# Kernel optimization log

Measured on AMD Instinct MI355X. Metric: run time of the kernel, lower is better.

## Reference

```python
import jax, jax.numpy as jnp
import numpy as np

B, LC, LQ, D, F = 16, 2048, 256, 768, 768
MASK_VALUE = -1.0e12


def setup_inputs() -> dict:
    key = jax.random.key(0)
    ks = jax.random.split(key, 6)
    scale = 1.0 / np.sqrt(D)
    return {
        "x_cont": jax.random.normal(ks[0], (B, LC, D), dtype=jnp.float32),
        "x_ques": jax.random.normal(ks[1], (B, LQ, D), dtype=jnp.float32),
        "ques_len": jax.random.randint(ks[2], (B, 1), 0, LQ, dtype=jnp.int32),
        "WC": jax.random.normal(ks[3], (D, F), dtype=jnp.float32) * scale,
        "WQ": jax.random.normal(ks[4], (D, F), dtype=jnp.float32) * scale,
        "V": jax.random.normal(ks[5], (2 * D, F), dtype=jnp.float32) * scale,
    }


def _mask_logits(logits, ques_len):
    # Original: one_hot(ques_len[:,0], Lq) -> 1 - cumsum along Lq -> tile over Lc.
    # mask[b, j] = 1 if j < ques_len[b] else 0.
    lq = logits.shape[-1]
    oh = jax.nn.one_hot(ques_len[:, 0], lq, dtype=jnp.float32)  # [B, Lq]
    valid = 1.0 - jnp.cumsum(oh, axis=1)                         # [B, Lq]
    return logits + MASK_VALUE * (1.0 - valid)[:, None, :]       # broadcast over Lc


def reference(x_cont, x_ques, ques_len, WC, WQ, V):
    filters = WC.shape[-1]
    x_cont_ = jax.nn.relu(jnp.einsum("bcd,df->bcf", x_cont, WC))  # [B, Lc, F]
    x_ques_ = jax.nn.relu(jnp.einsum("bqd,df->bqf", x_ques, WQ))  # [B, Lq, F]
    logits = jnp.einsum("bcf,bqf->bcq", x_cont_, x_ques_) / jnp.sqrt(
        jnp.asarray(filters, dtype=x_cont.dtype)
    )  # [B, Lc, Lq]
    logits = _mask_logits(logits, ques_len)
    attn = jax.nn.softmax(logits, axis=-1)
    C = jnp.einsum("bcq,bqd->bcd", attn, x_ques)                  # [B, Lc, D]
    res = jnp.concatenate([x_cont, C], axis=2)                    # [B, Lc, 2D]
    gate = jax.nn.sigmoid(jnp.einsum("bce,ef->bcf", res, V))      # [B, Lc, F]
    return gate
```

## Files before the change

### kernel.cpp

```cpp
#include <hip/hip_runtime.h>
#include <hip/hip_bf16.h>
#include <cstdint>


using bf16 = __hip_bfloat16;
typedef __attribute__((ext_vector_type(8))) __bf16 bf16x8;
typedef __attribute__((ext_vector_type(4))) float f32x4;

typedef __attribute__((address_space(1))) const uint32_t GU32;
typedef __attribute__((address_space(3))) uint32_t LU32;

__device__ __forceinline__ void gll16(const bf16* g, bf16* l) {
  __builtin_amdgcn_global_load_lds((GU32*)g, (LU32*)l, 16, 0, 0);
}
__device__ __forceinline__ f32x4 mfma_bf16(bf16x8 a, bf16x8 b, f32x4 c) {
  return __builtin_amdgcn_mfma_f32_16x16x32_bf16(a, b, c, 0, 0, 0);
}
__device__ __forceinline__ bf16x8 ld_frag(const bf16* p) {
  return *reinterpret_cast<const bf16x8*>(p);
}
__device__ __forceinline__ int swz(int r) { return (r & 3) ^ ((r >> 2) & 1); }

__device__ __forceinline__ unsigned short f2bf_bits(float x) {
  bf16 b = __float2bfloat16(x);
  union { bf16 b; unsigned short s; } u;
  u.b = b;
  return u.s;
}

__global__ void transpose4(const float* __restrict__ s0, const float* __restrict__ s1,
                           const float* __restrict__ s2, const float* __restrict__ s3,
                           bf16* __restrict__ d0, bf16* __restrict__ d1,
                           bf16* __restrict__ d2, bf16* __restrict__ d3) {
  __shared__ float tile[32][33];
  const int z = blockIdx.z;
  const float* in = (z == 0) ? s0 : (z == 1) ? s1 : (z == 2) ? s2 : s3;
  bf16* out = (z == 0) ? d0 : (z == 1) ? d1 : (z == 2) ? d2 : d3;
  int c0 = blockIdx.x * 32, r0 = blockIdx.y * 32;
  int tx = threadIdx.x, ty = threadIdx.y;
#pragma unroll
  for (int i = ty; i < 32; i += 8)
    tile[i][tx] = in[(long)(r0 + i) * 768 + (c0 + tx)];
  __syncthreads();
#pragma unroll
  for (int i = ty; i < 32; i += 8)
    out[(long)(c0 + i) * 768 + (r0 + tx)] = __float2bfloat16(tile[tx][i]);
}

__global__ void transpose_bf16(const bf16* __restrict__ in, bf16* __restrict__ out,
                               int R, int C, long ibs, long obs) {
  __shared__ bf16 tile[32][33];
  const bf16* inb = in + (long)blockIdx.z * ibs;
  bf16* outb = out + (long)blockIdx.z * obs;
  int c0 = blockIdx.x * 32, r0 = blockIdx.y * 32;
  int tx = threadIdx.x, ty = threadIdx.y;
#pragma unroll
  for (int i = ty; i < 32; i += 8)
    tile[i][tx] = inb[(long)(r0 + i) * C + (c0 + tx)];
  __syncthreads();
#pragma unroll
  for (int i = ty; i < 32; i += 8)
    outb[(long)(c0 + i) * R + (r0 + tx)] = tile[tx][i];
}

__global__ void convert_flat(const float* __restrict__ in, bf16* __restrict__ out, long n4) {
  long i = (long)blockIdx.x * blockDim.x + threadIdx.x;
  if (i >= n4) return;
  float4 v = reinterpret_cast<const float4*>(in)[i];
  ushort4 o;
  o.x = f2bf_bits(v.x);
  o.y = f2bf_bits(v.y);
  o.z = f2bf_bits(v.z);
  o.w = f2bf_bits(v.w);
  reinterpret_cast<ushort4*>(out)[i] = o;
}

__global__ __launch_bounds__(256) void gemm_bt_split(
    const bf16* __restrict__ A, long lda,
    const bf16* __restrict__ Bt, long ldb,
    bf16* __restrict__ O1, bf16* __restrict__ O2, int K) {
  __shared__ __align__(16) bf16 As[128 * 32];
  __shared__ __align__(16) bf16 Bs[128 * 32];
  const int tid = threadIdx.x;
  const int wave = tid >> 6;
  const int lane = tid & 63;
  const int l16 = lane & 15;
  const int kh = lane >> 4;
  const int wm = (wave >> 1) * 64;
  const int wn = (wave & 1) * 64;
  const long row0 = (long)blockIdx.x * 128;
  const long col0 = (long)blockIdx.y * 128;
  const int srow = tid >> 2;
  const int scol = ((tid & 3) ^ swz(srow)) * 8;

  const bf16* ap0 = A + (row0 + srow) * lda + scol;
  const bf16* ap1 = ap0 + 64 * lda;
  const bf16* bp0 = Bt + (col0 + srow) * ldb + scol;
  const bf16* bp1 = bp0 + 64 * ldb;
  bf16* as0 = As + wave * 512;
  bf16* as1 = as0 + 2048;
  bf16* bs0 = Bs + wave * 512;
  bf16* bs1 = bs0 + 2048;

  const int xc = (kh ^ swz(l16)) * 8;
  f32x4 acc[4][4] = {};

  for (int k0 = 0; k0 < K; k0 += 32) {
    gll16(ap0 + k0, as0);
    gll16(ap1 + k0, as1);
    gll16(bp0 + k0, bs0);
    gll16(bp1 + k0, bs1);
    __syncthreads();
    bf16x8 af[4], bfr[4];
#pragma unroll
    for (int i = 0; i < 4; ++i)
      af[i] = ld_frag(As + (wm + i * 16 + l16) * 32 + xc);
#pragma unroll
    for (int j = 0; j < 4; ++j)
      bfr[j] = ld_frag(Bs + (wn + j * 16 + l16) * 32 + xc);
#pragma unroll
    for (int i = 0; i < 4; ++i)
#pragma unroll
      for (int j = 0; j < 4; ++j)
        acc[i][j] = mfma_bf16(af[i], bfr[j], acc[i][j]);
    __syncthreads();
  }

  const bool isO1 = col0 < 768;
#pragma unroll
  for (int i = 0; i < 4; ++i)
#pragma unroll
    for (int j = 0; j < 4; ++j)
#pragma unroll
      for (int r = 0; r < 4; ++r) {
        long row = row0 + wm + i * 16 + kh * 4 + r;
        long col = col0 + wn + j * 16 + l16;
        float v = acc[i][j][r];
        if (isO1)
          O1[row * 768 + col] = __float2bfloat16(fmaxf(v, 0.0f));
        else
          O2[row * 768 + (col - 768)] = __float2bfloat16(v);
      }
}

__global__ __launch_bounds__(512, 2) void gemm4b(
    const bf16* __restrict__ A, long lda,
    const bf16* __restrict__ Bt, long ldb,
    bf16* __restrict__ O1, bf16* __restrict__ O2, int K) {
  extern __shared__ __align__(16) bf16 smem[];
  const int tid = threadIdx.x;
  const int wid = tid >> 6;
  const int lane = tid & 63;
  const int l15 = lane & 15;
  const int g = lane >> 4;
  const int wm = wid >> 2;
  const int wn = wid & 3;

  const int lin = blockIdx.x;
  const int per = (int)gridDim.x >> 3;
  const int wgid = (lin & 7) * per + (lin >> 3);
  const long row0 = (long)(wgid / 6) * 256;
  const long col0 = (long)(wgid % 6) * 256;

  const int srow = lane >> 2;
  const int sc = ((lane & 3) ^ swz(srow)) * 8;
  const int w16 = wid * 16;
  const bf16* Ab = A + (row0 + srow) * lda + sc;
  const bf16* Bb = Bt + (col0 + srow) * ldb + sc;

  f32x4 acc[8][4] = {};

  auto stageA = [&](int buf, int kk) {
    bf16* d = smem + buf * 16384 + w16 * 32;
    gll16(Ab + (long)w16 * lda + kk, d);
    gll16(Ab + (long)(128 + w16) * lda + kk, d + 128 * 32);
  };
  auto stageB = [&](int buf, int kk) {
    bf16* d = smem + buf * 16384 + 8192 + w16 * 32;
    gll16(Bb + (long)w16 * ldb + kk, d);
    gll16(Bb + (long)(128 + w16) * ldb + kk, d + 128 * 32);
  };
  const int xc = (g ^ swz(l15)) * 8;
  auto ldA = [&](int buf, int m) {
    int row = wm * 128 + m * 16 + l15;
    return ld_frag(smem + buf * 16384 + row * 32 + xc);
  };
  auto ldB = [&](int buf, int n) {
    int row = wn * 64 + n * 16 + l15;
    return ld_frag(smem + buf * 16384 + 8192 + row * 32 + xc);
  };

  stageA(0, 0);
  stageB(0, 0);
  stageA(1, 32);
  stageB(1, 32);
  stageA(2, 64);
  stageB(2, 64);
  asm volatile("s_waitcnt vmcnt(8)\n\ts_barrier" ::: "memory");

  const int NT = K >> 5;
  bf16x8 av[4], bv[4];

  for (int t = 0; t < NT; ++t) {
    const int cur = t & 3;
    const int pfb = (t + 3) & 3;
    const bool pf = (t + 3) < NT;
    const int kk = (t + 3) << 5;

#pragma unroll
    for (int n = 0; n < 4; ++n) bv[n] = ldB(cur, n);
#pragma unroll
    for (int m = 0; m < 4; ++m) av[m] = ldA(cur, m);
    if (pf) stageA(pfb, kk);
    __builtin_amdgcn_s_barrier();
    __builtin_amdgcn_s_setprio(1);
#pragma unroll
    for (int m = 0; m < 4; ++m)
#pragma unroll
      for (int n = 0; n < 4; ++n) acc[m][n] = mfma_bf16(av[m], bv[n], acc[m][n]);
    __builtin_amdgcn_s_setprio(0);
    __builtin_amdgcn_s_barrier();

#pragma unroll
    for (int m = 0; m < 4; ++m) av[m] = ldA(cur, 4 + m);
    if (pf) stageB(pfb, kk);
    __builtin_amdgcn_s_barrier();
    __builtin_amdgcn_s_setprio(1);
#pragma unroll
    for (int m = 0; m < 4; ++m)
#pragma unroll
      for (int n = 0; n < 4; ++n)
        acc[4 + m][n] = mfma_bf16(av[m], bv[n], acc[4 + m][n]);
    __builtin_amdgcn_s_setprio(0);

    if (t <= NT - 4)
      asm volatile("s_waitcnt vmcnt(8)\n\ts_barrier" ::: "memory");
    else if (t == NT - 3)
      asm volatile("s_waitcnt vmcnt(4)\n\ts_barrier" ::: "memory");
    else if (t == NT - 2)
      asm volatile("s_waitcnt vmcnt(0)\n\ts_barrier" ::: "memory");
  }

  const bool isO1 = col0 < 768;
#pragma unroll
  for (int m = 0; m < 8; ++m)
#pragma unroll
    for (int n = 0; n < 4; ++n)
#pragma unroll
      for (int r = 0; r < 4; ++r) {
        long row = row0 + wm * 128 + m * 16 + g * 4 + r;
        long col = col0 + wn * 64 + n * 16 + l15;
        float v = acc[m][n][r];
        if (isO1)
          O1[row * 768 + col] = __float2bfloat16(fmaxf(v, 0.0f));
        else
          O2[row * 768 + (col - 768)] = __float2bfloat16(v);
      }
}

__global__ __launch_bounds__(256) void attn_kernel(
    const bf16* __restrict__ xcW, const bf16* __restrict__ xqW,
    const bf16* __restrict__ xqVT, const bf16* __restrict__ G1,
    const int* __restrict__ qlen_arr, float* __restrict__ out) {
  extern __shared__ __align__(16) bf16 smem[];
  bf16* P = smem + 20480;
  float* wred = (float*)(smem + 37376);
  float* wsum = wred + 256;

  const int n = blockIdx.x;
  const int b = n & 15;
  const int ct = n >> 4;

  const int tid = threadIdx.x;
  const int wc = tid >> 6;
  const int lane = tid & 63;
  const int l16 = lane & 15;
  const int kh = lane >> 4;

  const int qlen = qlen_arr[b];
  const int qeff = (qlen == 0) ? 256 : qlen;
  const bool active = (wc * 64) < qeff;
  const int kkmax = (qeff + 31) >> 5;

  const long crow0 = (long)b * 2048 + (long)ct * 64;
  const int srow = lane >> 2;
  const int sc = ((lane & 3) ^ swz(srow)) * 8;
  const int xcr = (kh ^ swz(l16)) * 8;

  const bf16* ap = xcW + (crow0 + wc * 16 + srow) * 768 + sc;
  const bf16* bp = xqW + ((long)b * 256 + wc * 64 + srow) * 768 + sc;

  auto stage = [&](int bufi, int k0) {
    gll16(ap + k0, smem + bufi * 2048 + wc * 512);
    if (active) {
      bf16* bd = smem + 4096 + bufi * 8192 + wc * 2048;
#pragma unroll
      for (int q = 0; q < 4; ++q)
        gll16(bp + q * 16 * 768 + k0, bd + q * 512);
    }
  };

  f32x4 acc[4][4] = {};
  stage(0, 0);

  for (int t = 0; t < 24; ++t) {
    const int cur = t & 1;
    if (t + 1 < 24) {
      stage(cur ^ 1, (t + 1) * 32);
      if (active)
        asm volatile("s_waitcnt vmcnt(5)" ::: "memory");
      else
        asm volatile("s_waitcnt vmcnt(1)" ::: "memory");
      __builtin_amdgcn_s_barrier();
    } else {
      asm volatile("s_waitcnt vmcnt(0)\n\ts_barrier" ::: "memory");
    }
    if (active) {
      const bf16* Ac = smem + cur * 2048;
      const bf16* Bc = smem + 4096 + cur * 8192;
      bf16x8 af[4], bfr[4];
#pragma unroll
      for (int i = 0; i < 4; ++i)
        af[i] = ld_frag(Ac + (i * 16 + l16) * 32 + xcr);
#pragma unroll
      for (int j = 0; j < 4; ++j)
        bfr[j] = ld_frag(Bc + (wc * 64 + j * 16 + l16) * 32 + xcr);
      __builtin_amdgcn_s_setprio(1);
#pragma unroll
      for (int i = 0; i < 4; ++i)
#pragma unroll
        for (int j = 0; j < 4; ++j)
          acc[i][j] = mfma_bf16(af[i], bfr[j], acc[i][j]);
      __builtin_amdgcn_s_setprio(0);
    }
    __builtin_amdgcn_s_barrier();
  }

  const float scale = 0.036084391824351615f;

  if (active) {
#pragma unroll
    for (int i = 0; i < 4; ++i)
#pragma unroll
      for (int j = 0; j < 4; ++j) {
        int col = wc * 64 + j * 16 + l16;
        float m = (col >= qeff) ? -1.0e12f : 0.0f;
#pragma unroll
        for (int r = 0; r < 4; ++r)
          acc[i][j][r] = acc[i][j][r] * scale + m;
      }
#pragma unroll
    for (int i = 0; i < 4; ++i)
#pragma unroll
      for (int r = 0; r < 4; ++r) {
        float mx = fmaxf(fmaxf(acc[i][0][r], acc[i][1][r]),
                         fmaxf(acc[i][2][r], acc[i][3][r]));
        mx = fmaxf(mx, __shfl_xor(mx, 1));
        mx = fmaxf(mx, __shfl_xor(mx, 2));
        mx = fmaxf(mx, __shfl_xor(mx, 4));
        mx = fmaxf(mx, __shfl_xor(mx, 8));
        if (l16 == 0) wred[(i * 16 + kh * 4 + r) * 4 + wc] = mx;
      }
  } else if (l16 == 0) {
#pragma unroll
    for (int i = 0; i < 4; ++i)
#pragma unroll
      for (int r = 0; r < 4; ++r)
        wred[(i * 16 + kh * 4 + r) * 4 + wc] = -3.0e38f;
  }
  __syncthreads();

  if (active) {
#pragma unroll
    for (int i = 0; i < 4; ++i)
#pragma unroll
      for (int r = 0; r < 4; ++r) {
        int row = i * 16 + kh * 4 + r;
        float gm = fmaxf(fmaxf(wred[row * 4 + 0], wred[row * 4 + 1]),
                         fmaxf(wred[row * 4 + 2], wred[row * 4 + 3]));
        float s = 0.0f;
#pragma unroll
        for (int j = 0; j < 4; ++j) {
          float e = expf(acc[i][j][r] - gm);
          acc[i][j][r] = e;
          s += e;
        }
        s += __shfl_xor(s, 1);
        s += __shfl_xor(s, 2);
        s += __shfl_xor(s, 4);
        s += __shfl_xor(s, 8);
        if (l16 == 0) wsum[row * 4 + wc] = s;
      }
  } else if (l16 == 0) {
#pragma unroll
    for (int i = 0; i < 4; ++i)
#pragma unroll
      for (int r = 0; r < 4; ++r)
        wsum[(i * 16 + kh * 4 + r) * 4 + wc] = 0.0f;
  }
  __syncthreads();

  if (active) {
#pragma unroll
    for (int i = 0; i < 4; ++i)
#pragma unroll
      for (int r = 0; r < 4; ++r) {
        int row = i * 16 + kh * 4 + r;
        float inv = 1.0f / (wsum[row * 4 + 0] + wsum[row * 4 + 1] +
                            wsum[row * 4 + 2] + wsum[row * 4 + 3]);
#pragma unroll
        for (int j = 0; j < 4; ++j)
          P[row * 264 + wc * 64 + j * 16 + l16] = __float2bfloat16(acc[i][j][r] * inv);
      }
  }
  __syncthreads();

  bf16x8 pf[4][8];
#pragma unroll
  for (int kk = 0; kk < 8; ++kk) {
    if (kk >= kkmax) break;
#pragma unroll
    for (int i = 0; i < 4; ++i)
      pf[i][kk] = ld_frag(P + (i * 16 + l16) * 264 + kk * 32 + kh * 8);
  }

  for (int nb = 0; nb < 3; ++nb) {
    const int n0 = nb * 256 + wc * 64;
    const bf16* btp = xqVT + ((long)b * 768 + n0) * 256;
    f32x4 a2[4][4] = {};
#pragma unroll
    for (int kk = 0; kk < 8; ++kk) {
      if (kk >= kkmax) break;
      bf16x8 vf[4];
#pragma unroll
      for (int j = 0; j < 4; ++j)
        vf[j] = ld_frag(btp + (j * 16 + l16) * 256 + kk * 32 + kh * 8);
#pragma unroll
      for (int i = 0; i < 4; ++i)
#pragma unroll
        for (int j = 0; j < 4; ++j)
          a2[i][j] = mfma_bf16(pf[i][kk], vf[j], a2[i][j]);
    }
#pragma unroll
    for (int i = 0; i < 4; ++i)
#pragma unroll
      for (int j = 0; j < 4; ++j)
#pragma unroll
        for (int r = 0; r < 4; ++r) {
          long row = crow0 + i * 16 + kh * 4 + r;
          int col = n0 + j * 16 + l16;
          float v = a2[i][j][r] + __bfloat162float(G1[row * 768 + col]);
          out[row * 768 + col] = 1.0f / (1.0f + __expf(-v));
        }
  }
}

extern "C" void kernel_launch(void* const* d_in, const int* in_sizes, int n_in,
                              void* d_out, int out_size, void* d_ws, size_t ws_size,
                              hipStream_t stream) {
  const float* x_cont = (const float*)d_in[0];
  const float* x_ques = (const float*)d_in[1];
  const int* ques_len = (const int*)d_in[2];
  const float* WC = (const float*)d_in[3];
  const float* WQ = (const float*)d_in[4];
  const float* V = (const float*)d_in[5];
  float* out = (float*)d_out;

  bf16* Wct = (bf16*)d_ws;
  bf16* Wqt = Wct + (long)1536 * 768;
  bf16* xcB = Wqt + (long)1536 * 768;
  bf16* xqB = xcB + (long)32768 * 768;
  bf16* xcW = xqB + (long)4096 * 768;
  bf16* xqW = xcW + (long)32768 * 768;
  bf16* xqV = xqW + (long)4096 * 768;
  bf16* xqVT = xqV + (long)4096 * 768;
  bf16* G1 = xqVT + (long)16 * 768 * 256;

  (void)hipFuncSetAttribute(reinterpret_cast<const void*>(&gemm4b),
                            hipFuncAttributeMaxDynamicSharedMemorySize, 131072);
  (void)hipFuncSetAttribute(reinterpret_cast<const void*>(&attn_kernel),
                            hipFuncAttributeMaxDynamicSharedMemorySize, 76800);

  transpose4<<<dim3(24, 24, 4), dim3(32, 8), 0, stream>>>(
      WC, WQ, V, V + (long)768 * 768,
      Wct, Wqt, Wct + (long)768 * 768, Wqt + (long)768 * 768);

  convert_flat<<<24576, 256, 0, stream>>>(x_cont, xcB, (long)32768 * 768 / 4);
  convert_flat<<<3072, 256, 0, stream>>>(x_ques, xqB, (long)4096 * 768 / 4);

  gemm_bt_split<<<dim3(32, 12), 256, 0, stream>>>(xqB, 768, Wqt, 768, xqW, xqV, 768);
  transpose_bf16<<<dim3(24, 8, 16), dim3(32, 8), 0, stream>>>(
      xqV, xqVT, 256, 768, (long)256 * 768, (long)768 * 256);

  gemm4b<<<768, 512, 131072, stream>>>(xcB, 768, Wct, 768, xcW, G1, 768);

  attn_kernel<<<512, 256, 76800, stream>>>(xcW, xqW, xqVT, G1, ques_len, out);
}
```

Measured before the change: 264.9 us.

## Load attention operands directly into registers and remap blocks per XCD

The attention kernel no longer stages xcW/xqW tiles through LDS with async global-to-LDS loads and barriers. Each wave now double-buffers MFMA fragments straight from global memory into registers. Blocks are remapped so each XCD handles two batches, aiming for better L2 locality, and the convert kernel becomes grid-stride with fewer blocks. In exchange, the per-wave skipping of masked question columns (active/kkmax) is dropped, so work no longer scales with ques_len, and the four waves redundantly fetch the same A rows from global memory.

```diff
diff --git a/kernel.cpp b/kernel.cpp
--- a/kernel.cpp
+++ b/kernel.cpp
@@ -64,15 +64,16 @@
 }
 
 __global__ void convert_flat(const float* __restrict__ in, bf16* __restrict__ out, long n4) {
-  long i = (long)blockIdx.x * blockDim.x + threadIdx.x;
-  if (i >= n4) return;
-  float4 v = reinterpret_cast<const float4*>(in)[i];
-  ushort4 o;
-  o.x = f2bf_bits(v.x);
-  o.y = f2bf_bits(v.y);
-  o.z = f2bf_bits(v.z);
-  o.w = f2bf_bits(v.w);
-  reinterpret_cast<ushort4*>(out)[i] = o;
+  long stride = (long)gridDim.x * blockDim.x;
+  for (long i = (long)blockIdx.x * blockDim.x + threadIdx.x; i < n4; i += stride) {
+    float4 v = reinterpret_cast<const float4*>(in)[i];
+    ushort4 o;
+    o.x = f2bf_bits(v.x);
+    o.y = f2bf_bits(v.y);
+    o.z = f2bf_bits(v.z);
+    o.w = f2bf_bits(v.w);
+    reinterpret_cast<ushort4*>(out)[i] = o;
+  }
 }
 
 __global__ __launch_bounds__(256) void gemm_bt_split(
@@ -258,18 +259,20 @@
       }
 }
 
-__global__ __launch_bounds__(256) void attn_kernel(
+__global__ __launch_bounds__(256) void attn4(
     const bf16* __restrict__ xcW, const bf16* __restrict__ xqW,
     const bf16* __restrict__ xqVT, const bf16* __restrict__ G1,
     const int* __restrict__ qlen_arr, float* __restrict__ out) {
   extern __shared__ __align__(16) bf16 smem[];
-  bf16* P = smem + 20480;
-  float* wred = (float*)(smem + 37376);
+  bf16* P = smem;
+  float* wred = (float*)(smem + 33792);
   float* wsum = wred + 256;
 
-  const int n = blockIdx.x;
-  const int b = n & 15;
-  const int ct = n >> 4;
+  const int lin = blockIdx.x;
+  const int xcd = lin & 7;
+  const int jj = lin >> 3;
+  const int b = xcd * 2 + (jj >> 5);
+  const int ct = jj & 31;
 
   const int tid = threadIdx.x;
   const int wc = tid >> 6;
@@ -277,152 +280,119 @@
   const int l16 = lane & 15;
   const int kh = lane >> 4;
 
+  const long crow0 = (long)b * 2048 + (long)ct * 64;
+  const bf16* Ap = xcW + (crow0 + l16) * 768 + kh * 8;
+  const bf16* Bp = xqW + ((long)b * 256 + wc * 64 + l16) * 768 + kh * 8;
+
+  bf16x8 a0[4], b0[4], a1[4], b1[4];
+#pragma unroll
+  for (int i = 0; i < 4; ++i) a0[i] = ld_frag(Ap + i * 16 * 768);
+#pragma unroll
+  for (int j = 0; j < 4; ++j) b0[j] = ld_frag(Bp + j * 16 * 768);
+
+  f32x4 acc[4][4] = {};
+  for (int t = 0; t < 24; t += 2) {
+    if (t + 1 < 24) {
+      const bf16* ap = Ap + (t + 1) * 32;
+      const bf16* bp = Bp + (t + 1) * 32;
+#pragma unroll
+      for (int i = 0; i < 4; ++i) a1[i] = ld_frag(ap + i * 16 * 768);
+#pragma unroll
+      for (int j = 0; j < 4; ++j) b1[j] = ld_frag(bp + j * 16 * 768);
+    }
+    __builtin_amdgcn_s_setprio(1);
+#pragma unroll
+    for (int i = 0; i < 4; ++i)
+#pragma unroll
+      for (int j = 0; j < 4; ++j)
+        acc[i][j] = mfma_bf16(a0[i], b0[j], acc[i][j]);
+    __builtin_amdgcn_s_setprio(0);
+    if (t + 2 < 24) {
+      const bf16* ap = Ap + (t + 2) * 32;
+      const bf16* bp = Bp + (t + 2) * 32;
+#pragma unroll
+      for (int i = 0; i < 4; ++i) a0[i] = ld_frag(ap + i * 16 * 768);
+#pragma unroll
+      for (int j = 0; j < 4; ++j) b0[j] = ld_frag(bp + j * 16 * 768);
+    }
+    __builtin_amdgcn_s_setprio(1);
+#pragma unroll
+    for (int i = 0; i < 4; ++i)
+#pragma unroll
+      for (int j = 0; j < 4; ++j)
+        acc[i][j] = mfma_bf16(a1[i], b1[j], acc[i][j]);
+    __builtin_amdgcn_s_setprio(0);
+  }
+
+  const float scale = 0.036084391824351615f;
   const int qlen = qlen_arr[b];
-  const int qeff = (qlen == 0) ? 256 : qlen;
-  const bool active = (wc * 64) < qeff;
-  const int kkmax = (qeff + 31) >> 5;
-
-  const long crow0 = (long)b * 2048 + (long)ct * 64;
-  const int srow = lane >> 2;
-  const int sc = ((lane & 3) ^ swz(srow)) * 8;
-  const int xcr = (kh ^ swz(l16)) * 8;
-
-  const bf16* ap = xcW + (crow0 + wc * 16 + srow) * 768 + sc;
-  const bf16* bp = xqW + ((long)b * 256 + wc * 64 + srow) * 768 + sc;
-
-  auto stage = [&](int bufi, int k0) {
-    gll16(ap + k0, smem + bufi * 2048 + wc * 512);
-    if (active) {
-      bf16* bd = smem + 4096 + bufi * 8192 + wc * 2048;
-#pragma unroll
-      for (int q = 0; q < 4; ++q)
-        gll16(bp + q * 16 * 768 + k0, bd + q * 512);
-    }
-  };
-
-  f32x4 acc[4][4] = {};
-  stage(0, 0);
-
-  for (int t = 0; t < 24; ++t) {
-    const int cur = t & 1;
-    if (t + 1 < 24) {
-      stage(cur ^ 1, (t + 1) * 32);
-      if (active)
-        asm volatile("s_waitcnt vmcnt(5)" ::: "memory");
-      else
-        asm volatile("s_waitcnt vmcnt(1)" ::: "memory");
-      __builtin_amdgcn_s_barrier();
-    } else {
-      asm volatile("s_waitcnt vmcnt(0)\n\ts_barrier" ::: "memory");
-    }
-    if (active) {
-      const bf16* Ac = smem + cur * 2048;
-      const bf16* Bc = smem + 4096 + cur * 8192;
-      bf16x8 af[4], bfr[4];
-#pragma unroll
-      for (int i = 0; i < 4; ++i)
-        af[i] = ld_frag(Ac + (i * 16 + l16) * 32 + xcr);
-#pragma unroll
-      for (int j = 0; j < 4; ++j)
-        bfr[j] = ld_frag(Bc + (wc * 64 + j * 16 + l16) * 32 + xcr);
-      __builtin_amdgcn_s_setprio(1);
-#pragma unroll
-      for (int i = 0; i < 4; ++i)
-#pragma unroll
-        for (int j = 0; j < 4; ++j)
-          acc[i][j] = mfma_bf16(af[i], bfr[j], acc[i][j]);
-      __builtin_amdgcn_s_setprio(0);
-    }
-    __builtin_amdgcn_s_barrier();
-  }
-
-  const float scale = 0.036084391824351615f;
-
-  if (active) {
-#pragma unroll
-    for (int i = 0; i < 4; ++i)
+
+#pragma unroll
+  for (int i = 0; i < 4; ++i)
+#pragma unroll
+    for (int j = 0; j < 4; ++j) {
+      int col = wc * 64 + j * 16 + l16;
+      float m = (col >= qlen) ? -1.0e12f : 0.0f;
+#pragma unroll
+      for (int r = 0; r < 4; ++r)
+        acc[i][j][r] = acc[i][j][r] * scale + m;
+    }
+
+#pragma unroll
+  for (int i = 0; i < 4; ++i)
+#pragma unroll
+    for (int r = 0; r < 4; ++r) {
+      float mx = fmaxf(fmaxf(acc[i][0][r], acc[i][1][r]),
+                       fmaxf(acc[i][2][r], acc[i][3][r]));
+      mx = fmaxf(mx, __shfl_xor(mx, 1));
+      mx = fmaxf(mx, __shfl_xor(mx, 2));
+      mx = fmaxf(mx, __shfl_xor(mx, 4));
+      mx = fmaxf(mx, __shfl_xor(mx, 8));
+      if (l16 == 0) wred[(i * 16 + kh * 4 + r) * 4 + wc] = mx;
+    }
+  __syncthreads();
+
+#pragma unroll
+  for (int i = 0; i < 4; ++i)
+#pragma unroll
+    for (int r = 0; r < 4; ++r) {
+      int row = i * 16 + kh * 4 + r;
+      float gm = fmaxf(fmaxf(wred[row * 4 + 0], wred[row * 4 + 1]),
+                       fmaxf(wred[row * 4 + 2], wred[row * 4 + 3]));
+      float s = 0.0f;
 #pragma unroll
       for (int j = 0; j < 4; ++j) {
-        int col = wc * 64 + j * 16 + l16;
-        float m = (col >= qeff) ? -1.0e12f : 0.0f;
-#pragma unroll
-        for (int r = 0; r < 4; ++r)
-          acc[i][j][r] = acc[i][j][r] * scale + m;
+        float e = expf(acc[i][j][r] - gm);
+        acc[i][j][r] = e;
+        s += e;
       }
-#pragma unroll
-    for (int i = 0; i < 4; ++i)
-#pragma unroll
-      for (int r = 0; r < 4; ++r) {
-        float mx = fmaxf(fmaxf(acc[i][0][r], acc[i][1][r]),
-                         fmaxf(acc[i][2][r], acc[i][3][r]));
-        mx = fmaxf(mx, __shfl_xor(mx, 1));
-        mx = fmaxf(mx, __shfl_xor(mx, 2));
-        mx = fmaxf(mx, __shfl_xor(mx, 4));
-        mx = fmaxf(mx, __shfl_xor(mx, 8));
-        if (l16 == 0) wred[(i * 16 + kh * 4 + r) * 4 + wc] = mx;
-      }
-  } else if (l16 == 0) {
-#pragma unroll
-    for (int i = 0; i < 4; ++i)
-#pragma unroll
-      for (int r = 0; r < 4; ++r)
-        wred[(i * 16 + kh * 4 + r) * 4 + wc] = -3.0e38f;
-  }
+      s += __shfl_xor(s, 1);
+      s += __shfl_xor(s, 2);
+      s += __shfl_xor(s, 4);
+      s += __shfl_xor(s, 8);
+      if (l16 == 0) wsum[row * 4 + wc] = s;
+    }
   __syncthreads();
 
-  if (active) {
-#pragma unroll
-    for (int i = 0; i < 4; ++i)
-#pragma unroll
-      for (int r = 0; r < 4; ++r) {
-        int row = i * 16 + kh * 4 + r;
-        float gm = fmaxf(fmaxf(wred[row * 4 + 0], wred[row * 4 + 1]),
-                         fmaxf(wred[row * 4 + 2], wred[row * 4 + 3]));
-        float s = 0.0f;
-#pragma unroll
-        for (int j = 0; j < 4; ++j) {
-          float e = expf(acc[i][j][r] - gm);
-          acc[i][j][r] = e;
-          s += e;
-        }
-        s += __shfl_xor(s, 1);
-        s += __shfl_xor(s, 2);
-        s += __shfl_xor(s, 4);
-        s += __shfl_xor(s, 8);
-        if (l16 == 0) wsum[row * 4 + wc] = s;
-      }
-  } else if (l16 == 0) {
-#pragma unroll
-    for (int i = 0; i < 4; ++i)
-#pragma unroll
-      for (int r = 0; r < 4; ++r)
-        wsum[(i * 16 + kh * 4 + r) * 4 + wc] = 0.0f;
-  }
+#pragma unroll
+  for (int i = 0; i < 4; ++i)
+#pragma unroll
+    for (int r = 0; r < 4; ++r) {
+      int row = i * 16 + kh * 4 + r;
+      float inv = 1.0f / (wsum[row * 4 + 0] + wsum[row * 4 + 1] +
+                          wsum[row * 4 + 2] + wsum[row * 4 + 3]);
+#pragma unroll
+      for (int j = 0; j < 4; ++j)
+        P[row * 264 + wc * 64 + j * 16 + l16] = __float2bfloat16(acc[i][j][r] * inv);
+    }
   __syncthreads();
 
-  if (active) {
-#pragma unroll
-    for (int i = 0; i < 4; ++i)
-#pragma unroll
-      for (int r = 0; r < 4; ++r) {
-        int row = i * 16 + kh * 4 + r;
-        float inv = 1.0f / (wsum[row * 4 + 0] + wsum[row * 4 + 1] +
-                            wsum[row * 4 + 2] + wsum[row * 4 + 3]);
-#pragma unroll
-        for (int j = 0; j < 4; ++j)
-          P[row * 264 + wc * 64 + j * 16 + l16] = __float2bfloat16(acc[i][j][r] * inv);
-      }
-  }
-  __syncthreads();
-
   bf16x8 pf[4][8];
 #pragma unroll
-  for (int kk = 0; kk < 8; ++kk) {
-    if (kk >= kkmax) break;
-#pragma unroll
-    for (int i = 0; i < 4; ++i)
+  for (int i = 0; i < 4; ++i)
+#pragma unroll
+    for (int kk = 0; kk < 8; ++kk)
       pf[i][kk] = ld_frag(P + (i * 16 + l16) * 264 + kk * 32 + kh * 8);
-  }
 
   for (int nb = 0; nb < 3; ++nb) {
     const int n0 = nb * 256 + wc * 64;
@@ -430,7 +400,6 @@
     f32x4 a2[4][4] = {};
 #pragma unroll
     for (int kk = 0; kk < 8; ++kk) {
-      if (kk >= kkmax) break;
       bf16x8 vf[4];
 #pragma unroll
       for (int j = 0; j < 4; ++j)
@@ -478,15 +447,15 @@
 
   (void)hipFuncSetAttribute(reinterpret_cast<const void*>(&gemm4b),
                             hipFuncAttributeMaxDynamicSharedMemorySize, 131072);
-  (void)hipFuncSetAttribute(reinterpret_cast<const void*>(&attn_kernel),
-                            hipFuncAttributeMaxDynamicSharedMemorySize, 76800);
+  (void)hipFuncSetAttribute(reinterpret_cast<const void*>(&attn4),
+                            hipFuncAttributeMaxDynamicSharedMemorySize, 69632);
 
   transpose4<<<dim3(24, 24, 4), dim3(32, 8), 0, stream>>>(
       WC, WQ, V, V + (long)768 * 768,
       Wct, Wqt, Wct + (long)768 * 768, Wqt + (long)768 * 768);
 
-  convert_flat<<<24576, 256, 0, stream>>>(x_cont, xcB, (long)32768 * 768 / 4);
-  convert_flat<<<3072, 256, 0, stream>>>(x_ques, xqB, (long)4096 * 768 / 4);
+  convert_flat<<<3072, 256, 0, stream>>>(x_cont, xcB, (long)32768 * 768 / 4);
+  convert_flat<<<768, 256, 0, stream>>>(x_ques, xqB, (long)4096 * 768 / 4);
 
   gemm_bt_split<<<dim3(32, 12), 256, 0, stream>>>(xqB, 768, Wqt, 768, xqW, xqV, 768);
   transpose_bf16<<<dim3(24, 8, 16), dim3(32, 8), 0, stream>>>(
@@ -494,5 +463,5 @@
 
   gemm4b<<<768, 512, 131072, stream>>>(xcB, 768, Wct, 768, xcW, G1, 768);
 
-  attn_kernel<<<512, 256, 76800, stream>>>(xcW, xqW, xqVT, G1, ques_len, out);
-}
+  attn4<<<512, 256, 69632, stream>>>(xcW, xqW, xqVT, G1, ques_len, out);
+}
```

Measured after the change: 289.0 us. 9.1% more time.
